# Performance work log

Measured on AMD Instinct MI355X. Metric: run time of the kernel, lower is better.

Reference implementation:

```python
import jax, jax.numpy as jnp
import numpy as np

H = 64          # hidden_feats
NODE_IN = 128
EDGE_IN = 16
N_NODES = 40000
N_EDGES = 80000
N_GRAPHS = 256
READOUT = 1024
N_MP = 3        # num_step_message_passing
N_S2S = 3       # num_step_set2set


def setup_inputs() -> dict:
    key = jax.random.key(0)
    ks = jax.random.split(key, 12)
    s = 0.05
    return {
        "node_feats": jax.random.normal(ks[0], (N_NODES, NODE_IN), jnp.float32),
        "edge_feats": jax.random.normal(ks[1], (N_EDGES, EDGE_IN), jnp.float32),
        "edge_src": jax.random.randint(ks[2], (N_EDGES,), 0, N_NODES, dtype=jnp.int32),
        "edge_dst": jax.random.randint(ks[3], (N_EDGES,), 0, N_NODES, dtype=jnp.int32),
        # evenly partition nodes into graphs (sorted, every graph non-empty)
        "node_graph_ids": (jnp.arange(N_NODES) * N_GRAPHS // N_NODES).astype(jnp.int32),
        # project_node_feats: Linear(node_in, H)
        "W_proj": jax.random.normal(ks[4], (H, NODE_IN), jnp.float32) * s,
        "b_proj": jnp.zeros((H,), jnp.float32),
        # edge network: Linear(edge_in, H*H)
        "W_edge": jax.random.normal(ks[5], (H * H, EDGE_IN), jnp.float32) * s,
        "b_edge": jnp.zeros((H * H,), jnp.float32),
        # NNConv bias
        "b_conv": jnp.zeros((H,), jnp.float32),
        # GRU(H, H), torch gate order r|z|n
        "gru_W_ih": jax.random.normal(ks[6], (3 * H, H), jnp.float32) * s,
        "gru_W_hh": jax.random.normal(ks[7], (3 * H, H), jnp.float32) * s,
        "gru_b_ih": jnp.zeros((3 * H,), jnp.float32),
        "gru_b_hh": jnp.zeros((3 * H,), jnp.float32),
        # Set2Set LSTM(input=4H, hidden=2H), torch gate order i|f|g|o
        "lstm_W_ih": jax.random.normal(ks[8], (8 * H, 4 * H), jnp.float32) * s,
        "lstm_W_hh": jax.random.normal(ks[9], (8 * H, 2 * H), jnp.float32) * s,
        "lstm_b_ih": jnp.zeros((8 * H,), jnp.float32),
        "lstm_b_hh": jnp.zeros((8 * H,), jnp.float32),
        # sparsify: Linear(4H, READOUT) + PReLU (single param, init 0.25)
        "W_sp": jax.random.normal(ks[10], (READOUT, 4 * H), jnp.float32) * s,
        "b_sp": jnp.zeros((READOUT,), jnp.float32),
        "prelu_w": jnp.array(0.25, jnp.float32),
    }


def _forward(node_feats, edge_feats, edge_src, edge_dst, node_graph_ids,
             W_proj, b_proj, W_edge, b_edge, b_conv,
             gru_W_ih, gru_W_hh, gru_b_ih, gru_b_hh,
             lstm_W_ih, lstm_W_hh, lstm_b_ih, lstm_b_hh,
             W_sp, b_sp, prelu_w):
    N = node_feats.shape[0]
    x0 = jax.nn.relu(node_feats @ W_proj.T + b_proj)            # (N, H)
    # edge-conditioned weights (computed once; torch recomputes identically per step)
    We = (edge_feats @ W_edge.T + b_edge).reshape(-1, H, H)     # (E, H, H)
    x, hid = x0, x0                                             # GRU h0 = projected node feats
    for _ in range(N_MP):
        # NNConv: gather src feats, per-edge matmul, scatter-sum to dst
        msg = jnp.einsum('eh,eho->eo', x[edge_src], We)         # (E, H)
        agg = jax.ops.segment_sum(msg, edge_dst, num_segments=N) + b_conv
        a = jax.nn.relu(agg)
        # GRUCell (seq_len=1)
        gi = a @ gru_W_ih.T + gru_b_ih
        gh = hid @ gru_W_hh.T + gru_b_hh
        i_r, i_z, i_n = jnp.split(gi, 3, axis=-1)
        h_r, h_z, h_n = jnp.split(gh, 3, axis=-1)
        r = jax.nn.sigmoid(i_r + h_r)
        z = jax.nn.sigmoid(i_z + h_z)
        n = jnp.tanh(i_n + r * h_n)
        hid = (1.0 - z) * n + z * hid
        x = hid
    feat = jnp.concatenate([x0, x], axis=1)                     # (N, 2H)
    D = 2 * H
    B = N_GRAPHS
    # Set2Set pooling
    q_star = jnp.zeros((B, 2 * D), feat.dtype)
    h_l = jnp.zeros((B, D), feat.dtype)
    c_l = jnp.zeros((B, D), feat.dtype)
    for _ in range(N_S2S):
        gates = q_star @ lstm_W_ih.T + lstm_b_ih + h_l @ lstm_W_hh.T + lstm_b_hh
        i_g, f_g, g_g, o_g = jnp.split(gates, 4, axis=-1)
        c_l = jax.nn.sigmoid(f_g) * c_l + jax.nn.sigmoid(i_g) * jnp.tanh(g_g)
        h_l = jax.nn.sigmoid(o_g) * jnp.tanh(c_l)
        q = h_l                                                 # (B, D)
        e = jnp.sum(feat * q[node_graph_ids], axis=-1)          # (N,)
        # segment softmax (every graph is non-empty by construction)
        e_max = jax.ops.segment_max(e, node_graph_ids, num_segments=B)
        ex = jnp.exp(e - e_max[node_graph_ids])
        denom = jax.ops.segment_sum(ex, node_graph_ids, num_segments=B)
        alpha = ex / denom[node_graph_ids]
        r_b = jax.ops.segment_sum(alpha[:, None] * feat, node_graph_ids, num_segments=B)
        q_star = jnp.concatenate([q, r_b], axis=-1)             # (B, 2D)
    out = q_star @ W_sp.T + b_sp                                # (B, READOUT)
    return jnp.where(out >= 0, out, prelu_w * out)              # PReLU


def reference(node_feats, edge_feats, edge_src, edge_dst, node_graph_ids,
              W_proj, b_proj, W_edge, b_edge, b_conv,
              gru_W_ih, gru_W_hh, gru_b_ih, gru_b_hh,
              lstm_W_ih, lstm_W_hh, lstm_b_ih, lstm_b_hh,
              W_sp, b_sp, prelu_w):
    return _forward(node_feats, edge_feats, edge_src, edge_dst, node_graph_ids,
                    W_proj, b_proj, W_edge, b_edge, b_conv,
                    gru_W_ih, gru_W_hh, gru_b_ih, gru_b_hh,
                    lstm_W_ih, lstm_W_hh, lstm_b_ih, lstm_b_hh,
                    W_sp, b_sp, prelu_w)
```

## Files before the change

kernel.cpp:

```cpp
#include <hip/hip_runtime.h>
#include <math.h>

#define H 64
#define NODE_IN 128
#define EDGE_IN 16
#define N_NODES 40000
#define N_EDGES 80000
#define N_GRAPHS 256
#define READOUT 1024
#define D2 128
#define QS 256

typedef unsigned short u16;
typedef __attribute__((ext_vector_type(8))) short bf16x8;
typedef __attribute__((ext_vector_type(4))) float f32x4;
#define MFMA16(a,b,c) __builtin_amdgcn_mfma_f32_16x16x32_bf16(a,b,c,0,0,0)

__device__ u16 d_xhi[N_NODES*H];
__device__ u16 d_xlo[N_NODES*H];
__device__ u16 d_efh[N_EDGES*EDGE_IN];
__device__ u16 d_weF[17*4*2*64*8];
__device__ u16 d_bcF[4*16*64*8];
__device__ float d_wspT[256*1024];

__device__ __forceinline__ float sigmoidf_(float x){ return 1.0f/(1.0f + expf(-x)); }

__device__ __forceinline__ u16 bf_hi(float x){
  union { float f; unsigned u; } c; c.f = x;
  unsigned r = (c.u + 0x7FFFu + ((c.u >> 16) & 1u)) >> 16;
  return (u16)r;
}
__device__ __forceinline__ float bf_f(u16 h){
  union { unsigned u; float f; } c; c.u = ((unsigned)h) << 16; return c.f;
}
__device__ __forceinline__ u16 bf_lo(float x, u16 hi){ return bf_hi(x - bf_f(hi)); }

__device__ __forceinline__ bf16x8 rne8(const float* Z){
  union { bf16x8 v; u16 u[8]; } hh;
  #pragma unroll
  for (int k = 0; k < 8; ++k) hh.u[k] = bf_hi(Z[k]);
  return hh.v;
}

__global__ __launch_bounds__(256) void pack_weF(
    const float* __restrict__ We, const float* __restrict__ be){
  int i = blockIdx.x*256 + threadIdx.x;
  int j = i & 7, lane = (i >> 3) & 63, half = (i >> 9) & 1;
  int nt = (i >> 10) & 3, ci = i >> 12;
  int o = nt*16 + (lane & 15);
  int c = ci*64 + half*32 + (lane >> 4)*8 + j;
  float v = (c < 1024) ? We[(size_t)((c >> 4)*64 + o)*EDGE_IN + (c & 15)]
                       : be[(size_t)(c - 1024)*64 + o];
  d_weF[i] = bf_hi(v);
}

__global__ __launch_bounds__(256) void pack_bcF(
    const float* __restrict__ Wih, const float* __restrict__ Whh){
  int i = blockIdx.x*256 + threadIdx.x;
  int j = i & 7, lane = (i >> 3) & 63, nt = (i >> 9) & 15, kc = i >> 13;
  int cr = nt*16 + (lane & 15);
  int k  = kc*32 + (lane >> 4)*8 + j;
  float v;
  if (cr < 128){
    v = (k < 64) ? Wih[(size_t)cr*H + k] : Whh[(size_t)cr*H + (k-64)];
  } else if (cr < 192){
    int d = cr - 128;
    v = (k < 64) ? Wih[(size_t)(128+d)*H + k] : 0.f;
  } else {
    int d = cr - 192;
    v = (k < 64) ? 0.f : Whh[(size_t)(128+d)*H + (k-64)];
  }
  d_bcF[i] = bf_hi(v);
}

__global__ __launch_bounds__(256) void pack_wspT(const float* __restrict__ Wsp){
  int i = blockIdx.x*256 + threadIdx.x;
  int j = i >> 8, k = i & 255;
  d_wspT[(size_t)k*1024 + j] = Wsp[i];
}

__global__ __launch_bounds__(256) void pack_efh(const float* __restrict__ ef){
  int i = blockIdx.x*256 + threadIdx.x;
  d_efh[i] = bf_hi(ef[i]);
}

__global__ __launch_bounds__(256) void zero_buf(float4* __restrict__ p, int n4){
  int i = blockIdx.x*256 + threadIdx.x;
  int stride = gridDim.x*256;
  for (; i < n4; i += stride) p[i] = make_float4(0.f,0.f,0.f,0.f);
}

__global__ __launch_bounds__(256) void proj_mm(
    const float* __restrict__ nf, const float* __restrict__ Wp,
    const float* __restrict__ bp, float* __restrict__ x0, float* __restrict__ h){
  __shared__ float A_s[NODE_IN][64];
  __shared__ float B_s[NODE_IN][64];
  int t = threadIdx.x;
  int nb = blockIdx.x * 64;
  #pragma unroll
  for (int p = 0; p < 8; ++p){
    int idx = p*256 + t;
    int n = idx >> 5, k4 = idx & 31;
    float4 v = ((const float4*)(nf + (size_t)(nb+n)*NODE_IN))[k4];
    int base = (((n>>2) ^ (k4 & 15)) << 2) + (n & 3);
    A_s[k4*4+0][base]=v.x; A_s[k4*4+1][base]=v.y;
    A_s[k4*4+2][base]=v.z; A_s[k4*4+3][base]=v.w;
  }
  #pragma unroll
  for (int p = 0; p < 8; ++p){
    int idx = p*256 + t;
    int c = idx & 63, k4 = idx >> 6;
    float4 v = ((const float4*)(Wp + (size_t)c*NODE_IN))[k4];
    B_s[k4*4+0][c]=v.x; B_s[k4*4+1][c]=v.y; B_s[k4*4+2][c]=v.z; B_s[k4*4+3][c]=v.w;
  }
  __syncthreads();
  int eg = t & 15, cg = t >> 4;
  float acc[4][4] = {};
  #pragma unroll 4
  for (int k = 0; k < NODE_IN; ++k){
    int s = (k >> 2) & 15;
    float4 a = *(const float4*)&A_s[k][(eg ^ s) << 2];
    float4 b = *(const float4*)&B_s[k][cg*4];
    float av[4] = {a.x,a.y,a.z,a.w};
    float bv[4] = {b.x,b.y,b.z,b.w};
    #pragma unroll
    for (int j = 0; j < 4; ++j)
      #pragma unroll
      for (int c = 0; c < 4; ++c) acc[j][c] += av[j]*bv[c];
  }
  float4 bb = ((const float4*)bp)[cg];
  float bv[4] = {bb.x,bb.y,bb.z,bb.w};
  #pragma unroll
  for (int j = 0; j < 4; ++j){
    int n = nb + eg*4 + j;
    float o[4];
    #pragma unroll
    for (int c = 0; c < 4; ++c) o[c] = fmaxf(acc[j][c]+bv[c], 0.f);
    *(float4*)(x0 + (size_t)n*H + cg*4) = make_float4(o[0],o[1],o[2],o[3]);
    *(float4*)(h  + (size_t)n*H + cg*4) = make_float4(o[0],o[1],o[2],o[3]);
    u16 hs[4], ls[4];
    #pragma unroll
    for (int c = 0; c < 4; ++c){ hs[c] = bf_hi(o[c]); ls[c] = bf_lo(o[c], hs[c]); }
    *(ushort4*)&d_xhi[(size_t)n*H + cg*4] = make_ushort4(hs[0],hs[1],hs[2],hs[3]);
    *(ushort4*)&d_xlo[(size_t)n*H + cg*4] = make_ushort4(ls[0],ls[1],ls[2],ls[3]);
  }
}

__global__ __launch_bounds__(256) void edge_mfma(
    const int* __restrict__ src, const int* __restrict__ dst,
    float* __restrict__ agg){
  __shared__ __align__(16) float x_s[64][68];
  int t = threadIdx.x;
  int w = t >> 6, lane = t & 63;
  int m = lane & 15, kq = lane >> 4;
  int ebase = blockIdx.x * 64;
  int e0 = t >> 2, j4 = t & 3;
  {
    int s0 = src[ebase + e0];
    const bf16x8* ph = (const bf16x8*)&d_xhi[(size_t)s0*H + j4*16];
    union { bf16x8 v; u16 u[8]; } a, b;
    a.v = ph[0]; b.v = ph[1];
    float* xr = &x_s[e0][j4*16];
    #pragma unroll
    for (int j = 0; j < 8; ++j){
      xr[j]     = bf_f(a.u[j]);
      xr[8 + j] = bf_f(b.u[j]);
    }
  }
  int e = w*16 + m;
  float ef8[8];
  {
    const bf16x8* p = (const bf16x8*)&d_efh[(size_t)(ebase+e)*EDGE_IN + (kq&1)*8];
    union { bf16x8 v; u16 u[8]; } t8; t8.v = p[0];
    #pragma unroll
    for (int j = 0; j < 8; ++j) ef8[j] = bf_f(t8.u[j]);
  }
  int hsel = kq >> 1;
  const bf16x8* wF = (const bf16x8*)d_weF + lane;
  f32x4 acc[4];
  #pragma unroll
  for (int i = 0; i < 4; ++i) acc[i] = (f32x4){0.f,0.f,0.f,0.f};

  #pragma unroll 2
  for (int ci = 0; ci < 16; ++ci){
    float x0v = x_s[e][ci*4 + hsel];
    float x1v = x_s[e][ci*4 + 2 + hsel];
    float Z0[8], Z1[8];
    #pragma unroll
    for (int j = 0; j < 8; ++j){ Z0[j] = x0v*ef8[j]; Z1[j] = x1v*ef8[j]; }
    bf16x8 a0 = rne8(Z0), a1 = rne8(Z1);
    #pragma unroll
    for (int nt = 0; nt < 4; ++nt){
      bf16x8 b0 = wF[(size_t)((ci*4+nt)*2 + 0)*64];
      bf16x8 b1 = wF[(size_t)((ci*4+nt)*2 + 1)*64];
      acc[nt] = MFMA16(a0, b0, acc[nt]);
      acc[nt] = MFMA16(a1, b1, acc[nt]);
    }
  }
  {
    float xb[16];
    {
      const float4* q0 = (const float4*)&x_s[e][kq*8];
      const float4* q1 = (const float4*)&x_s[e][32 + kq*8];
      float4 a=q0[0], b=q0[1], c=q1[0], d=q1[1];
      xb[0]=a.x; xb[1]=a.y; xb[2]=a.z; xb[3]=a.w;
      xb[4]=b.x; xb[5]=b.y; xb[6]=b.z; xb[7]=b.w;
      xb[8]=c.x; xb[9]=c.y; xb[10]=c.z; xb[11]=c.w;
      xb[12]=d.x; xb[13]=d.y; xb[14]=d.z; xb[15]=d.w;
    }
    bf16x8 a0 = rne8(xb), a1 = rne8(xb + 8);
    #pragma unroll
    for (int nt = 0; nt < 4; ++nt){
      bf16x8 b0 = wF[(size_t)((64+nt)*2 + 0)*64];
      bf16x8 b1 = wF[(size_t)((64+nt)*2 + 1)*64];
      acc[nt] = MFMA16(a0, b0, acc[nt]);
      acc[nt] = MFMA16(a1, b1, acc[nt]);
    }
  }
  float* msg_s = (float*)x_s;
  #pragma unroll
  for (int nt = 0; nt < 4; ++nt){
    int o = nt*16 + m;
    #pragma unroll
    for (int r = 0; r < 4; ++r){
      int ee = w*16 + kq*4 + r;
      msg_s[ee*68 + (o ^ ((ee & 7) << 2))] = acc[nt][r];
    }
  }
  #pragma unroll
  for (int r = 0; r < 16; ++r){
    int ee = w*16 + r;
    int dn = dst[ebase + ee];
    atomicAdd(&agg[(size_t)dn*H + lane],
              msg_s[ee*68 + (lane ^ ((ee & 7) << 2))]);
  }
}

__global__ __launch_bounds__(256) void gru_mm_mfma(
    float* __restrict__ agg, const float* __restrict__ bconv,
    float* __restrict__ h, const float* __restrict__ gbih,
    const float* __restrict__ gbhh){
  __shared__ u16 Ah[64][40], Al[64][40];
  __shared__ float bih_s[192], bhh_s[192];
  int t = threadIdx.x;
  int w = t >> 6, lane = t & 63;
  int nb = blockIdx.x * 64;
  if (t < 192){ bih_s[t] = gbih[t]; bhh_s[t] = gbhh[t]; }
  int m = lane & 15, kj = (lane >> 4) * 8;
  const bf16x8* bF = (const bf16x8*)d_bcF + lane;
  f32x4 acc[16];
  #pragma unroll
  for (int i = 0; i < 16; ++i) acc[i] = (f32x4){0.f,0.f,0.f,0.f};
  for (int kc = 0; kc < 4; ++kc){
    {
      int n = t >> 2, q = t & 3;
      if (kc < 2){
        float* sp = agg + (size_t)(nb+n)*H + kc*32 + q*8;
        float4 v0 = *(const float4*)sp;
        float4 v1 = *(const float4*)(sp + 4);
        float4 b0 = *(const float4*)&bconv[kc*32 + q*8];
        float4 b1 = *(const float4*)&bconv[kc*32 + q*8 + 4];
        *(float4*)sp       = make_float4(0.f,0.f,0.f,0.f);
        *(float4*)(sp + 4) = make_float4(0.f,0.f,0.f,0.f);
        float vals[8] = { fmaxf(v0.x+b0.x,0.f), fmaxf(v0.y+b0.y,0.f),
                          fmaxf(v0.z+b0.z,0.f), fmaxf(v0.w+b0.w,0.f),
                          fmaxf(v1.x+b1.x,0.f), fmaxf(v1.y+b1.y,0.f),
                          fmaxf(v1.z+b1.z,0.f), fmaxf(v1.w+b1.w,0.f) };
        union { bf16x8 v; u16 u[8]; } ph, pl;
        #pragma unroll
        for (int j = 0; j < 8; ++j){
          u16 hi = bf_hi(vals[j]);
          ph.u[j] = hi; pl.u[j] = bf_lo(vals[j], hi);
        }
        *(bf16x8*)&Ah[n][q*8] = ph.v;
        *(bf16x8*)&Al[n][q*8] = pl.v;
      } else {
        int gofs = (nb+n)*H + (kc-2)*32 + q*8;
        *(bf16x8*)&Ah[n][q*8] = *(const bf16x8*)&d_xhi[gofs];
        *(bf16x8*)&Al[n][q*8] = *(const bf16x8*)&d_xlo[gofs];
      }
    }
    bf16x8 ah = *(const bf16x8*)&Ah[w*16 + m][kj];
    bf16x8 al = *(const bf16x8*)&Al[w*16 + m][kj];
    #pragma unroll
    for (int nt = 0; nt < 16; ++nt){
      bf16x8 bh = bF[(size_t)(kc*16 + nt)*64];
      acc[nt] = MFMA16(ah, bh, acc[nt]);
      acc[nt] = MFMA16(al, bh, acc[nt]);
    }
  }
  __syncthreads();
  int q4 = lane >> 4, col0 = lane & 15;
  #pragma unroll
  for (int r = 0; r < 4; ++r){
    int node = nb + w*16 + q4*4 + r;
    #pragma unroll
    for (int j = 0; j < 4; ++j){
      int d = col0 + 16*j;
      float rg = sigmoidf_(acc[j][r]   + bih_s[d]      + bhh_s[d]);
      float z  = sigmoidf_(acc[4+j][r] + bih_s[64+d]   + bhh_s[64+d]);
      float nn = tanhf(acc[8+j][r] + bih_s[128+d] + rg*(acc[12+j][r] + bhh_s[128+d]));
      size_t off = (size_t)node*H + d;
      float hv = h[off];
      float hn = (1.f - z)*nn + z*hv;
      h[off] = hn;
      u16 hb = bf_hi(hn);
      d_xhi[off] = hb;
      d_xlo[off] = bf_lo(hn, hb);
    }
  }
}

__global__ __launch_bounds__(256) void build_bl2(
    const float* __restrict__ Wih, const float* __restrict__ Whh,
    float* __restrict__ Bl2){
  int i = blockIdx.x*256 + threadIdx.x;
  int k = i >> 9, c = i & 511;
  int d = c >> 2, gate = c & 3;
  int row = gate*128 + d;
  float v = (k < 256) ? Wih[(size_t)row*QS + k] : Whh[(size_t)row*D2 + (k-256)];
  Bl2[i] = v;
}

__global__ __launch_bounds__(512) void s2s_kernel(
    const float* __restrict__ x0, const float* __restrict__ h,
    const float* __restrict__ Bl2, const float* __restrict__ lbih,
    const float* __restrict__ lbhh, float* __restrict__ hl,
    float* __restrict__ cl, float* __restrict__ qstar){
  __shared__ float A_s[384];
  __shared__ float part4[4][128][4];
  __shared__ float q_s[D2];
  __shared__ float alpha_s[160];
  __shared__ float wred[8];
  __shared__ float part[8][D2];
  int g = blockIdx.x, t = threadIdx.x;
  int lane = t & 63, w = t >> 6;
  if (t < 384){
    A_s[t] = (t < 256) ? qstar[(size_t)g*QS + t] : hl[(size_t)g*D2 + (t - 256)];
  }
  __syncthreads();
  {
    int d = t & 127, ks = t >> 7;
    const float* bp = Bl2 + 4*d;
    float ai = 0.f, af = 0.f, ag = 0.f, ao = 0.f;
    #pragma unroll 8
    for (int kk = 0; kk < 96; ++kk){
      int k = ks*96 + kk;
      float a = A_s[k];
      float4 b = *(const float4*)(bp + (size_t)k*512);
      ai += a*b.x; af += a*b.y; ag += a*b.z; ao += a*b.w;
    }
    *(float4*)&part4[ks][d][0] = make_float4(ai, af, ag, ao);
  }
  __syncthreads();
  if (t < D2){
    float4 p0 = *(const float4*)&part4[0][t][0];
    float4 p1 = *(const float4*)&part4[1][t][0];
    float4 p2 = *(const float4*)&part4[2][t][0];
    float4 p3 = *(const float4*)&part4[3][t][0];
    float iv = p0.x+p1.x+p2.x+p3.x + lbih[t]       + lbhh[t];
    float fv = p0.y+p1.y+p2.y+p3.y + lbih[128 + t] + lbhh[128 + t];
    float gv = p0.z+p1.z+p2.z+p3.z + lbih[256 + t] + lbhh[256 + t];
    float ov = p0.w+p1.w+p2.w+p3.w + lbih[384 + t] + lbhh[384 + t];
    float c = sigmoidf_(fv)*cl[(size_t)g*D2 + t] + sigmoidf_(iv)*tanhf(gv);
    float hn = sigmoidf_(ov)*tanhf(c);
    cl[(size_t)g*D2 + t] = c;
    hl[(size_t)g*D2 + t] = hn;
    q_s[t] = hn;
  }
  __syncthreads();
  int n0 = (g*N_NODES + N_GRAPHS - 1)/N_GRAPHS;
  int n1 = ((g+1)*N_NODES + N_GRAPHS - 1)/N_GRAPHS;
  int cnt = n1 - n0;
  float e = -1e30f;
  if (t < cnt){
    int n = n0 + t;
    const float4* xr = (const float4*)(x0 + (size_t)n*H);
    const float4* hr = (const float4*)(h  + (size_t)n*H);
    const float4* q1 = (const float4*)q_s;
    const float4* q2 = (const float4*)(q_s + H);
    float s = 0.0f;
    #pragma unroll
    for (int k4 = 0; k4 < 16; ++k4){
      float4 a = xr[k4], b = q1[k4];
      s += a.x*b.x + a.y*b.y + a.z*b.z + a.w*b.w;
    }
    #pragma unroll
    for (int k4 = 0; k4 < 16; ++k4){
      float4 a = hr[k4], b = q2[k4];
      s += a.x*b.x + a.y*b.y + a.z*b.z + a.w*b.w;
    }
    e = s;
  }
  float mx = e;
  #pragma unroll
  for (int off = 32; off >= 1; off >>= 1) mx = fmaxf(mx, __shfl_xor(mx, off));
  if (lane == 0) wred[w] = mx;
  __syncthreads();
  float gm = wred[0];
  #pragma unroll
  for (int i = 1; i < 8; ++i) gm = fmaxf(gm, wred[i]);
  __syncthreads();
  float ex = (t < cnt) ? expf(e - gm) : 0.0f;
  float sm = ex;
  #pragma unroll
  for (int off = 32; off >= 1; off >>= 1) sm += __shfl_xor(sm, off);
  if (lane == 0) wred[w] = sm;
  __syncthreads();
  float denom = wred[0]+wred[1]+wred[2]+wred[3]+wred[4]+wred[5]+wred[6]+wred[7];
  if (t < cnt) alpha_s[t] = ex / denom;
  __syncthreads();
  float acc0 = 0.f, acc1 = 0.f;
  for (int i = w; i < cnt; i += 8){
    float a = alpha_s[i];
    acc0 += a * x0[(size_t)(n0+i)*H + lane];
    acc1 += a * h [(size_t)(n0+i)*H + lane];
  }
  part[w][lane]      = acc0;
  part[w][64 + lane] = acc1;
  __syncthreads();
  if (t < D2){
    float v = 0.f;
    #pragma unroll
    for (int i = 0; i < 8; ++i) v += part[i][t];
    qstar[(size_t)g*QS + t]      = q_s[t];
    qstar[(size_t)g*QS + D2 + t] = v;
  }
}

__global__ __launch_bounds__(256) void out_kernel(
    const float* __restrict__ qstar, const float* __restrict__ bsp,
    const float* __restrict__ prelu, float* __restrict__ out){
  __shared__ float q_s[QS];
  int g = blockIdx.x >> 1, half = blockIdx.x & 1;
  int t = threadIdx.x;
  q_s[t] = qstar[(size_t)g*QS + t];
  __syncthreads();
  int j0 = half*512 + t;
  float acc0 = bsp[j0], acc1 = bsp[j0 + 256];
  const float* wp = d_wspT + j0;
  #pragma unroll 4
  for (int k = 0; k < QS; ++k){
    float q = q_s[k];
    acc0 += q * wp[(size_t)k*1024];
    acc1 += q * wp[(size_t)k*1024 + 256];
  }
  float pw = prelu[0];
  out[(size_t)g*READOUT + j0]       = (acc0 >= 0.0f) ? acc0 : pw*acc0;
  out[(size_t)g*READOUT + j0 + 256] = (acc1 >= 0.0f) ? acc1 : pw*acc1;
}

extern "C" void kernel_launch(void* const* d_in, const int* in_sizes, int n_in,
                              void* d_out, int out_size, void* d_ws, size_t ws_size,
                              hipStream_t stream) {
  const float* node_feats = (const float*)d_in[0];
  const float* edge_feats = (const float*)d_in[1];
  const int*   esrc       = (const int*)d_in[2];
  const int*   edst       = (const int*)d_in[3];
  const float* Wproj = (const float*)d_in[5];
  const float* bproj = (const float*)d_in[6];
  const float* Wedge = (const float*)d_in[7];
  const float* bedge = (const float*)d_in[8];
  const float* bconv = (const float*)d_in[9];
  const float* gWih  = (const float*)d_in[10];
  const float* gWhh  = (const float*)d_in[11];
  const float* gbih  = (const float*)d_in[12];
  const float* gbhh  = (const float*)d_in[13];
  const float* lWih  = (const float*)d_in[14];
  const float* lWhh  = (const float*)d_in[15];
  const float* lbih  = (const float*)d_in[16];
  const float* lbhh  = (const float*)d_in[17];
  const float* Wsp   = (const float*)d_in[18];
  const float* bsp   = (const float*)d_in[19];
  const float* prelu = (const float*)d_in[20];

  float* ws    = (float*)d_ws;
  float* x0    = ws;
  float* h     = ws + 2560000;
  float* agg   = ws + 5120000;
  float* qstar = ws + 7680000;
  float* hl    = qstar + 65536;
  float* cl    = hl + 32768;
  float* Bl2   = agg;

  hipMemsetAsync(qstar, 0, (65536 + 32768 + 32768)*sizeof(float), stream);

  pack_weF<<<272, 256, 0, stream>>>(Wedge, bedge);
  pack_bcF<<<128, 256, 0, stream>>>(gWih, gWhh);
  pack_wspT<<<1024, 256, 0, stream>>>(Wsp);
  pack_efh<<<5000, 256, 0, stream>>>(edge_feats);

  proj_mm<<<N_NODES/64, 256, 0, stream>>>(node_feats, Wproj, bproj, x0, h);

  for (int s = 0; s < 3; ++s){
    if (s == 0)
      zero_buf<<<2048, 256, 0, stream>>>((float4*)agg, N_NODES*H/4);
    edge_mfma<<<N_EDGES/64, 256, 0, stream>>>(esrc, edst, agg);
    gru_mm_mfma<<<N_NODES/64, 256, 0, stream>>>(agg, bconv, h, gbih, gbhh);
  }

  build_bl2<<<768, 256, 0, stream>>>(lWih, lWhh, Bl2);

  for (int s = 0; s < 3; ++s){
    s2s_kernel<<<N_GRAPHS, 512, 0, stream>>>(x0, h, Bl2, lbih, lbhh, hl, cl, qstar);
  }

  out_kernel<<<2*N_GRAPHS, 256, 0, stream>>>(qstar, bsp, prelu, (float*)d_out);
}
```

Measured before the change: 314.0 us.

## Merge setup packing kernels, fold agg zeroing into proj, fuse readout into set2set

All weight and edge-feature packing kernels, the LSTM weight rebuild and the qstar/hl/cl memset are combined into one block-dispatched kernel. Bl2 moves to its own workspace region so it can be built early. Zeroing of the aggregation buffer rides on extra blocks of the projection kernel. The final readout linear plus PReLU is fused into the last set2set step. The aim is fewer launches and inter-kernel gaps, at the cost of a readout now spread over 256 blocks instead of 512, with each thread doing more serial work.

```diff
diff --git a/kernel.cpp b/kernel.cpp
--- a/kernel.cpp
+++ b/kernel.cpp
@@ -42,60 +42,72 @@
   return hh.v;
 }
 
-__global__ __launch_bounds__(256) void pack_weF(
-    const float* __restrict__ We, const float* __restrict__ be){
-  int i = blockIdx.x*256 + threadIdx.x;
-  int j = i & 7, lane = (i >> 3) & 63, half = (i >> 9) & 1;
-  int nt = (i >> 10) & 3, ci = i >> 12;
-  int o = nt*16 + (lane & 15);
-  int c = ci*64 + half*32 + (lane >> 4)*8 + j;
-  float v = (c < 1024) ? We[(size_t)((c >> 4)*64 + o)*EDGE_IN + (c & 15)]
-                       : be[(size_t)(c - 1024)*64 + o];
-  d_weF[i] = bf_hi(v);
-}
-
-__global__ __launch_bounds__(256) void pack_bcF(
-    const float* __restrict__ Wih, const float* __restrict__ Whh){
-  int i = blockIdx.x*256 + threadIdx.x;
-  int j = i & 7, lane = (i >> 3) & 63, nt = (i >> 9) & 15, kc = i >> 13;
-  int cr = nt*16 + (lane & 15);
-  int k  = kc*32 + (lane >> 4)*8 + j;
-  float v;
-  if (cr < 128){
-    v = (k < 64) ? Wih[(size_t)cr*H + k] : Whh[(size_t)cr*H + (k-64)];
-  } else if (cr < 192){
-    int d = cr - 128;
-    v = (k < 64) ? Wih[(size_t)(128+d)*H + k] : 0.f;
+__global__ __launch_bounds__(256) void mega_pack(
+    const float* __restrict__ We, const float* __restrict__ be,
+    const float* __restrict__ gWih, const float* __restrict__ gWhh,
+    const float* __restrict__ lWih, const float* __restrict__ lWhh,
+    const float* __restrict__ Wsp, const float* __restrict__ ef,
+    float* __restrict__ Bl2, float* __restrict__ qzero){
+  int b = blockIdx.x, t = threadIdx.x;
+  if (b < 5000){
+    int i = b*256 + t;
+    d_efh[i] = bf_hi(ef[i]);
+  } else if (b < 6024){
+    int i = (b-5000)*256 + t;
+    int j = i >> 8, k = i & 255;
+    d_wspT[(size_t)k*1024 + j] = Wsp[i];
+  } else if (b < 6792){
+    int i = (b-6024)*256 + t;
+    int k = i >> 9, c = i & 511;
+    int d = c >> 2, gate = c & 3;
+    int row = gate*128 + d;
+    Bl2[i] = (k < 256) ? lWih[(size_t)row*QS + k] : lWhh[(size_t)row*D2 + (k-256)];
+  } else if (b < 7064){
+    int i = (b-6792)*256 + t;
+    int j = i & 7, lane = (i >> 3) & 63, half = (i >> 9) & 1;
+    int nt = (i >> 10) & 3, ci = i >> 12;
+    int o = nt*16 + (lane & 15);
+    int c = ci*64 + half*32 + (lane >> 4)*8 + j;
+    float v = (c < 1024) ? We[(size_t)((c >> 4)*64 + o)*EDGE_IN + (c & 15)]
+                         : be[(size_t)(c - 1024)*64 + o];
+    d_weF[i] = bf_hi(v);
+  } else if (b < 7192){
+    int i = (b-7064)*256 + t;
+    int j = i & 7, lane = (i >> 3) & 63, nt = (i >> 9) & 15, kc = i >> 13;
+    int cr = nt*16 + (lane & 15);
+    int k  = kc*32 + (lane >> 4)*8 + j;
+    float v;
+    if (cr < 128){
+      v = (k < 64) ? gWih[(size_t)cr*H + k] : gWhh[(size_t)cr*H + (k-64)];
+    } else if (cr < 192){
+      int d = cr - 128;
+      v = (k < 64) ? gWih[(size_t)(128+d)*H + k] : 0.f;
+    } else {
+      int d = cr - 192;
+      v = (k < 64) ? 0.f : gWhh[(size_t)(128+d)*H + (k-64)];
+    }
+    d_bcF[i] = bf_hi(v);
   } else {
-    int d = cr - 192;
-    v = (k < 64) ? 0.f : Whh[(size_t)(128+d)*H + (k-64)];
-  }
-  d_bcF[i] = bf_hi(v);
-}
-
-__global__ __launch_bounds__(256) void pack_wspT(const float* __restrict__ Wsp){
-  int i = blockIdx.x*256 + threadIdx.x;
-  int j = i >> 8, k = i & 255;
-  d_wspT[(size_t)k*1024 + j] = Wsp[i];
-}
-
-__global__ __launch_bounds__(256) void pack_efh(const float* __restrict__ ef){
-  int i = blockIdx.x*256 + threadIdx.x;
-  d_efh[i] = bf_hi(ef[i]);
-}
-
-__global__ __launch_bounds__(256) void zero_buf(float4* __restrict__ p, int n4){
-  int i = blockIdx.x*256 + threadIdx.x;
-  int stride = gridDim.x*256;
-  for (; i < n4; i += stride) p[i] = make_float4(0.f,0.f,0.f,0.f);
+    int i = (b-7192)*256 + t;
+    ((float4*)qzero)[i] = make_float4(0.f,0.f,0.f,0.f);
+  }
 }
 
 __global__ __launch_bounds__(256) void proj_mm(
     const float* __restrict__ nf, const float* __restrict__ Wp,
-    const float* __restrict__ bp, float* __restrict__ x0, float* __restrict__ h){
+    const float* __restrict__ bp, float* __restrict__ x0, float* __restrict__ h,
+    float* __restrict__ aggz){
   __shared__ float A_s[NODE_IN][64];
   __shared__ float B_s[NODE_IN][64];
   int t = threadIdx.x;
+  if (blockIdx.x >= N_NODES/64){
+    int bb = blockIdx.x - N_NODES/64;
+    float4* p = (float4*)aggz;
+    int i0 = (bb*256 + t)*4;
+    #pragma unroll
+    for (int j = 0; j < 4; ++j) p[i0 + j] = make_float4(0.f,0.f,0.f,0.f);
+    return;
+  }
   int nb = blockIdx.x * 64;
   #pragma unroll
   for (int p = 0; p < 8; ++p){
@@ -311,22 +323,13 @@
   }
 }
 
-__global__ __launch_bounds__(256) void build_bl2(
-    const float* __restrict__ Wih, const float* __restrict__ Whh,
-    float* __restrict__ Bl2){
-  int i = blockIdx.x*256 + threadIdx.x;
-  int k = i >> 9, c = i & 511;
-  int d = c >> 2, gate = c & 3;
-  int row = gate*128 + d;
-  float v = (k < 256) ? Wih[(size_t)row*QS + k] : Whh[(size_t)row*D2 + (k-256)];
-  Bl2[i] = v;
-}
-
 __global__ __launch_bounds__(512) void s2s_kernel(
     const float* __restrict__ x0, const float* __restrict__ h,
     const float* __restrict__ Bl2, const float* __restrict__ lbih,
     const float* __restrict__ lbhh, float* __restrict__ hl,
-    float* __restrict__ cl, float* __restrict__ qstar){
+    float* __restrict__ cl, float* __restrict__ qstar,
+    const float* __restrict__ bsp, const float* __restrict__ prelu,
+    float* __restrict__ outp, int doOut){
   __shared__ float A_s[384];
   __shared__ float part4[4][128][4];
   __shared__ float q_s[D2];
@@ -425,29 +428,21 @@
     for (int i = 0; i < 8; ++i) v += part[i][t];
     qstar[(size_t)g*QS + t]      = q_s[t];
     qstar[(size_t)g*QS + D2 + t] = v;
-  }
-}
-
-__global__ __launch_bounds__(256) void out_kernel(
-    const float* __restrict__ qstar, const float* __restrict__ bsp,
-    const float* __restrict__ prelu, float* __restrict__ out){
-  __shared__ float q_s[QS];
-  int g = blockIdx.x >> 1, half = blockIdx.x & 1;
-  int t = threadIdx.x;
-  q_s[t] = qstar[(size_t)g*QS + t];
-  __syncthreads();
-  int j0 = half*512 + t;
-  float acc0 = bsp[j0], acc1 = bsp[j0 + 256];
-  const float* wp = d_wspT + j0;
-  #pragma unroll 4
-  for (int k = 0; k < QS; ++k){
-    float q = q_s[k];
-    acc0 += q * wp[(size_t)k*1024];
-    acc1 += q * wp[(size_t)k*1024 + 256];
-  }
-  float pw = prelu[0];
-  out[(size_t)g*READOUT + j0]       = (acc0 >= 0.0f) ? acc0 : pw*acc0;
-  out[(size_t)g*READOUT + j0 + 256] = (acc1 >= 0.0f) ? acc1 : pw*acc1;
+    if (doOut){ A_s[t] = q_s[t]; A_s[D2 + t] = v; }
+  }
+  if (doOut){
+    __syncthreads();
+    float pw = prelu[0];
+    #pragma unroll
+    for (int rep = 0; rep < 2; ++rep){
+      int j = rep*512 + t;
+      float acc = bsp[j];
+      #pragma unroll 4
+      for (int k = 0; k < QS; ++k)
+        acc += A_s[k] * d_wspT[(size_t)k*1024 + j];
+      outp[(size_t)g*READOUT + j] = (acc >= 0.0f) ? acc : pw*acc;
+    }
+  }
 }
 
 extern "C" void kernel_launch(void* const* d_in, const int* in_sizes, int n_in,
@@ -481,29 +476,21 @@
   float* qstar = ws + 7680000;
   float* hl    = qstar + 65536;
   float* cl    = hl + 32768;
-  float* Bl2   = agg;
-
-  hipMemsetAsync(qstar, 0, (65536 + 32768 + 32768)*sizeof(float), stream);
-
-  pack_weF<<<272, 256, 0, stream>>>(Wedge, bedge);
-  pack_bcF<<<128, 256, 0, stream>>>(gWih, gWhh);
-  pack_wspT<<<1024, 256, 0, stream>>>(Wsp);
-  pack_efh<<<5000, 256, 0, stream>>>(edge_feats);
-
-  proj_mm<<<N_NODES/64, 256, 0, stream>>>(node_feats, Wproj, bproj, x0, h);
+  float* Bl2   = cl + 32768;
+
+  mega_pack<<<7320, 256, 0, stream>>>(Wedge, bedge, gWih, gWhh, lWih, lWhh,
+                                      Wsp, edge_feats, Bl2, qstar);
+
+  proj_mm<<<2*(N_NODES/64), 256, 0, stream>>>(node_feats, Wproj, bproj, x0, h, agg);
 
   for (int s = 0; s < 3; ++s){
-    if (s == 0)
-      zero_buf<<<2048, 256, 0, stream>>>((float4*)agg, N_NODES*H/4);
     edge_mfma<<<N_EDGES/64, 256, 0, stream>>>(esrc, edst, agg);
     gru_mm_mfma<<<N_NODES/64, 256, 0, stream>>>(agg, bconv, h, gbih, gbhh);
   }
 
-  build_bl2<<<768, 256, 0, stream>>>(lWih, lWhh, Bl2);
-
   for (int s = 0; s < 3; ++s){
-    s2s_kernel<<<N_GRAPHS, 512, 0, stream>>>(x0, h, Bl2, lbih, lbhh, hl, cl, qstar);
-  }
-
-  out_kernel<<<2*N_GRAPHS, 256, 0, stream>>>(qstar, bsp, prelu, (float*)d_out);
-}
+    s2s_kernel<<<N_GRAPHS, 512, 0, stream>>>(x0, h, Bl2, lbih, lbhh, hl, cl,
+                                             qstar, bsp, prelu, (float*)d_out,
+                                             s == 2 ? 1 : 0);
+  }
+}
```

Result: no change. 316.4 us (+0.8%).
